# Optimization experiments

Hardware: AMD Instinct MI355X
Metric: run time of the kernel (lower is better)

Reference implementation:

```python
import jax, jax.numpy as jnp
import numpy as np

NUM_NODES = 500000
MEM_DIM = 172
BATCH = 4096


def setup_inputs() -> dict:
    key = jax.random.key(0)
    ks = jax.random.split(key, 8)
    s = 1.0 / np.sqrt(MEM_DIM)  # torch GRUCell init: U(-1/sqrt(hidden), 1/sqrt(hidden))
    return {
        "node_ids": jax.random.randint(ks[0], (BATCH,), 0, NUM_NODES),
        "messages": jax.random.normal(ks[1], (BATCH, MEM_DIM), dtype=jnp.float32),
        "timestamps": jax.random.uniform(ks[2], (BATCH,), dtype=jnp.float32),
        "memory": jax.random.normal(ks[3], (NUM_NODES, MEM_DIM), dtype=jnp.float32) * 0.1,
        "last_update": jnp.zeros((NUM_NODES,), dtype=jnp.float32),
        "w_ih": jax.random.uniform(ks[4], (3 * MEM_DIM, MEM_DIM), minval=-s, maxval=s, dtype=jnp.float32),
        "w_hh": jax.random.uniform(ks[5], (3 * MEM_DIM, MEM_DIM), minval=-s, maxval=s, dtype=jnp.float32),
        "b_ih": jax.random.uniform(ks[6], (3 * MEM_DIM,), minval=-s, maxval=s, dtype=jnp.float32),
        "b_hh": jax.random.uniform(ks[7], (3 * MEM_DIM,), minval=-s, maxval=s, dtype=jnp.float32),
    }


def _gru_cell(x, h, w_ih, w_hh, b_ih, b_hh):
    # torch.nn.GRUCell math. x, h: [B, D]; w_*: [3D, D]; b_*: [3D]
    gi = x @ w_ih.T + b_ih  # [B, 3D]
    gh = h @ w_hh.T + b_hh  # [B, 3D]
    i_r, i_z, i_n = jnp.split(gi, 3, axis=-1)
    h_r, h_z, h_n = jnp.split(gh, 3, axis=-1)
    r = jax.nn.sigmoid(i_r + h_r)
    z = jax.nn.sigmoid(i_z + h_z)
    n = jnp.tanh(i_n + r * h_n)
    return (1.0 - z) * n + z * h


def reference(node_ids, messages, timestamps, memory, last_update, w_ih, w_hh, b_ih, b_hh):
    # Gather current memory for the touched nodes
    current = memory[node_ids]  # [B, D]
    updated = _gru_cell(messages, current, w_ih, w_hh, b_ih, b_hh)  # [B, D]
    new_memory = memory.at[node_ids].set(updated)
    new_last_update = last_update.at[node_ids].set(timestamps)
    return new_memory, new_last_update
```

## Files before the change

### kernel.cpp

```cpp
#include <hip/hip_runtime.h>
#include <math.h>

#define D     172
#define D4    43
#define G3    516
#define RPB   8
#define TPB   256
#define NCOPY 2048
#define WT_HALF (43 * 516)
#define WT_F4   (2 * WT_HALF)

typedef float vfloat4 __attribute__((ext_vector_type(4)));

__global__ __launch_bounds__(256) void prep_kernel(const float* __restrict__ w_ih,
                                                   const float* __restrict__ w_hh,
                                                   float4* __restrict__ wt) {
    int idx = blockIdx.x * 256 + threadIdx.x;
    if (idx < WT_F4) {
        int m   = idx / WT_HALF;
        int rem = idx - m * WT_HALF;
        int k4  = rem / G3;
        int row = rem - k4 * G3;
        const float* src = m ? w_hh : w_ih;
        wt[idx] = *(const float4*)(src + (long)row * D + 4 * k4);
    }
}

__global__ __launch_bounds__(TPB) void copy_kernel(const vfloat4* __restrict__ mem4,
                                                   const vfloat4* __restrict__ lu4,
                                                   vfloat4* __restrict__ out4,
                                                   vfloat4* __restrict__ outlu4,
                                                   unsigned memf4, unsigned luf4) {
    const unsigned gid    = blockIdx.x * TPB + threadIdx.x;
    const unsigned stride = NCOPY * TPB;

    for (unsigned i0 = gid; i0 < memf4; i0 += 4u * stride) {
        unsigned i1 = i0 + stride, i2 = i0 + 2u * stride, i3 = i0 + 3u * stride;
        vfloat4 v0, v1, v2, v3;
        v0 = mem4[i0];
        if (i1 < memf4) v1 = mem4[i1];
        if (i2 < memf4) v2 = mem4[i2];
        if (i3 < memf4) v3 = mem4[i3];
        out4[i0] = v0;
        if (i1 < memf4) out4[i1] = v1;
        if (i2 < memf4) out4[i2] = v2;
        if (i3 < memf4) out4[i3] = v3;
    }
    if (gid < luf4) outlu4[gid] = lu4[gid];
}

__global__ __launch_bounds__(TPB) void gru_kernel(
    const int*   __restrict__ ids,  const float* __restrict__ msg,
    const float* __restrict__ ts,   const float* __restrict__ mem,
    const float* __restrict__ b_ih, const float* __restrict__ b_hh,
    const float4* __restrict__ wt,
    float* __restrict__ out_mem,    float* __restrict__ out_lu,
    int B) {

    __shared__ float4 sxh[2][RPB][D4];
    __shared__ int    s_id[RPB];
    __shared__ float  s_ts[RPB];
    __shared__ int    s_dup[RPB];

    const int tid  = threadIdx.x;
    const int base = blockIdx.x * RPB;

    if (tid < RPB) {
        s_id[tid]  = ids[base + tid];
        s_ts[tid]  = ts[base + tid];
        s_dup[tid] = 0;
    }
    __syncthreads();

    for (int it = tid; it < 2 * RPB * D4; it += TPB) {
        int which = it / (RPB * D4);
        int rem   = it - which * (RPB * D4);
        int r     = rem / D4;
        int k4    = rem - r * D4;
        const float* src = which ? (mem + (long)s_id[r] * D)
                                 : (msg + (long)(base + r) * D);
        ((float4*)sxh)[it] = *(const float4*)(src + 4 * k4);
    }
    for (int r = 0; r < RPB; ++r) {
        int my = s_id[r];
        for (int j = base + r + 1 + tid; j < B; j += TPB) {
            if (ids[j] == my) { s_dup[r] = 1; break; }
        }
    }
    __syncthreads();

    if (tid < D) {
        float acc[6][RPB];
        #pragma unroll
        for (int g = 0; g < 6; ++g)
            #pragma unroll
            for (int r = 0; r < RPB; ++r) acc[g][r] = 0.0f;

        const float4* wtB = wt + WT_HALF;
        for (int k4 = 0; k4 < D4; ++k4) {
            const int o = k4 * G3 + tid;
            float4 a0 = wt [o];
            float4 a1 = wt [o + D];
            float4 a2 = wt [o + 2 * D];
            float4 c0 = wtB[o];
            float4 c1 = wtB[o + D];
            float4 c2 = wtB[o + 2 * D];
            #pragma unroll
            for (int r = 0; r < RPB; ++r) {
                float4 xv = sxh[0][r][k4];
                float4 hv = sxh[1][r][k4];
                acc[0][r] += a0.x * xv.x + a0.y * xv.y + a0.z * xv.z + a0.w * xv.w;
                acc[1][r] += a1.x * xv.x + a1.y * xv.y + a1.z * xv.z + a1.w * xv.w;
                acc[2][r] += a2.x * xv.x + a2.y * xv.y + a2.z * xv.z + a2.w * xv.w;
                acc[3][r] += c0.x * hv.x + c0.y * hv.y + c0.z * hv.z + c0.w * hv.w;
                acc[4][r] += c1.x * hv.x + c1.y * hv.y + c1.z * hv.z + c1.w * hv.w;
                acc[5][r] += c2.x * hv.x + c2.y * hv.y + c2.z * hv.z + c2.w * hv.w;
            }
        }

        float bir = b_ih[tid], biz = b_ih[D + tid], bin_ = b_ih[2 * D + tid];
        float bhr = b_hh[tid], bhz = b_hh[D + tid], bhn  = b_hh[2 * D + tid];
        #pragma unroll
        for (int r = 0; r < RPB; ++r) {
            float i_r = acc[0][r] + bir;
            float i_z = acc[1][r] + biz;
            float i_n = acc[2][r] + bin_;
            float h_r = acc[3][r] + bhr;
            float h_z = acc[4][r] + bhz;
            float h_n = acc[5][r] + bhn;
            float rg = 1.0f / (1.0f + expf(-(i_r + h_r)));
            float zg = 1.0f / (1.0f + expf(-(i_z + h_z)));
            float ng = tanhf(i_n + rg * h_n);
            float hv = ((const float*)sxh[1][r])[tid];
            float outv = (1.0f - zg) * ng + zg * hv;
            if (!s_dup[r]) out_mem[(long)s_id[r] * D + tid] = outv;
        }
    }
    if (tid < RPB && !s_dup[tid]) out_lu[s_id[tid]] = s_ts[tid];
}

extern "C" void kernel_launch(void* const* d_in, const int* in_sizes, int n_in,
                              void* d_out, int out_size, void* d_ws, size_t ws_size,
                              hipStream_t stream) {
    const int*   node_ids    = (const int*)d_in[0];
    const float* messages    = (const float*)d_in[1];
    const float* timestamps  = (const float*)d_in[2];
    const float* memory      = (const float*)d_in[3];
    const float* last_update = (const float*)d_in[4];
    const float* w_ih        = (const float*)d_in[5];
    const float* w_hh        = (const float*)d_in[6];
    const float* b_ih        = (const float*)d_in[7];
    const float* b_hh        = (const float*)d_in[8];
    float* out = (float*)d_out;

    const int B = in_sizes[0];
    const int N = in_sizes[4];
    const long memf = (long)N * D;
    const unsigned memf4 = (unsigned)(memf / 4);
    const unsigned luf4  = (unsigned)(N / 4);

    float4* wt = (float4*)d_ws;

    prep_kernel<<<(WT_F4 + 255) / 256, 256, 0, stream>>>(w_ih, w_hh, wt);
    copy_kernel<<<NCOPY, TPB, 0, stream>>>((const vfloat4*)memory,
                                           (const vfloat4*)last_update,
                                           (vfloat4*)out,
                                           (vfloat4*)(out + memf),
                                           memf4, luf4);
    gru_kernel<<<B / RPB, TPB, 0, stream>>>(node_ids, messages, timestamps, memory,
                                            b_ih, b_hh, (const float4*)wt,
                                            out, out + memf, B);
}
```

Before: 225.1 us.

## Fuse GRU compute with bulk memory copy and scatter results in separate kernel

Runs the GRU matmul blocks and the large memory/last_update copy in one launch, so the compute-bound GRU work overlaps the bandwidth-bound copy instead of running after it. GRU outputs, ids, timestamps and duplicate flags go to a workspace, and a new scatter kernel writes them into the output after the copy finishes. The copy loop is simplified to a single strided load/store per iteration. A fallback path with a naive direct GRU kernel is added for when the workspace is too small. The cost is an extra kernel launch plus a round trip of the GRU results through global memory.

```diff
diff --git a/kernel.cpp b/kernel.cpp
--- a/kernel.cpp
+++ b/kernel.cpp
@@ -6,6 +6,7 @@
 #define G3    516
 #define RPB   8
 #define TPB   256
+#define NGRU  512
 #define NCOPY 2048
 #define WT_HALF (43 * 516)
 #define WT_F4   (2 * WT_HALF)
@@ -26,49 +27,29 @@
     }
 }
 
-__global__ __launch_bounds__(TPB) void copy_kernel(const vfloat4* __restrict__ mem4,
-                                                   const vfloat4* __restrict__ lu4,
-                                                   vfloat4* __restrict__ out4,
-                                                   vfloat4* __restrict__ outlu4,
-                                                   unsigned memf4, unsigned luf4) {
-    const unsigned gid    = blockIdx.x * TPB + threadIdx.x;
-    const unsigned stride = NCOPY * TPB;
-
-    for (unsigned i0 = gid; i0 < memf4; i0 += 4u * stride) {
-        unsigned i1 = i0 + stride, i2 = i0 + 2u * stride, i3 = i0 + 3u * stride;
-        vfloat4 v0, v1, v2, v3;
-        v0 = mem4[i0];
-        if (i1 < memf4) v1 = mem4[i1];
-        if (i2 < memf4) v2 = mem4[i2];
-        if (i3 < memf4) v3 = mem4[i3];
-        out4[i0] = v0;
-        if (i1 < memf4) out4[i1] = v1;
-        if (i2 < memf4) out4[i2] = v2;
-        if (i3 < memf4) out4[i3] = v3;
-    }
-    if (gid < luf4) outlu4[gid] = lu4[gid];
-}
-
-__global__ __launch_bounds__(TPB) void gru_kernel(
+__device__ __forceinline__ void gru_block(
+    int gblk,
     const int*   __restrict__ ids,  const float* __restrict__ msg,
     const float* __restrict__ ts,   const float* __restrict__ mem,
     const float* __restrict__ b_ih, const float* __restrict__ b_hh,
     const float4* __restrict__ wt,
-    float* __restrict__ out_mem,    float* __restrict__ out_lu,
+    float* __restrict__ gout, int* __restrict__ g_id,
+    float* __restrict__ g_ts, int* __restrict__ g_dup,
     int B) {
 
     __shared__ float4 sxh[2][RPB][D4];
     __shared__ int    s_id[RPB];
-    __shared__ float  s_ts[RPB];
     __shared__ int    s_dup[RPB];
 
     const int tid  = threadIdx.x;
-    const int base = blockIdx.x * RPB;
+    const int base = gblk * RPB;
 
     if (tid < RPB) {
-        s_id[tid]  = ids[base + tid];
-        s_ts[tid]  = ts[base + tid];
+        int id = ids[base + tid];
+        s_id[tid]  = id;
         s_dup[tid] = 0;
+        g_id[base + tid] = id;
+        g_ts[base + tid] = ts[base + tid];
     }
     __syncthreads();
 
@@ -88,6 +69,7 @@
         }
     }
     __syncthreads();
+    if (tid < RPB) g_dup[base + tid] = s_dup[tid];
 
     if (tid < D) {
         float acc[6][RPB];
@@ -132,11 +114,99 @@
             float zg = 1.0f / (1.0f + expf(-(i_z + h_z)));
             float ng = tanhf(i_n + rg * h_n);
             float hv = ((const float*)sxh[1][r])[tid];
-            float outv = (1.0f - zg) * ng + zg * hv;
-            if (!s_dup[r]) out_mem[(long)s_id[r] * D + tid] = outv;
-        }
-    }
-    if (tid < RPB && !s_dup[tid]) out_lu[s_id[tid]] = s_ts[tid];
+            gout[(long)(base + r) * D + tid] = (1.0f - zg) * ng + zg * hv;
+        }
+    }
+}
+
+__global__ __launch_bounds__(TPB) void fused_kernel(
+    const int*   __restrict__ ids,  const float* __restrict__ msg,
+    const float* __restrict__ ts,   const float* __restrict__ mem,
+    const float* __restrict__ lu,
+    const float* __restrict__ b_ih, const float* __restrict__ b_hh,
+    const float4* __restrict__ wt,
+    float* __restrict__ gout, int* __restrict__ g_id,
+    float* __restrict__ g_ts, int* __restrict__ g_dup,
+    float* __restrict__ out_mem,    float* __restrict__ out_lu,
+    int B, int N) {
+
+    if (blockIdx.x < NGRU) {
+        gru_block(blockIdx.x, ids, msg, ts, mem, b_ih, b_hh, wt,
+                  gout, g_id, g_ts, g_dup, B);
+        return;
+    }
+    const unsigned gid    = (blockIdx.x - NGRU) * TPB + threadIdx.x;
+    const unsigned stride = NCOPY * TPB;
+    const unsigned memf4  = (unsigned)N * D4;
+    const vfloat4* mem4 = (const vfloat4*)mem;
+    vfloat4* out4 = (vfloat4*)out_mem;
+    for (unsigned i = gid; i < memf4; i += stride) out4[i] = mem4[i];
+    const unsigned luf4 = (unsigned)N / 4;
+    const vfloat4* lu4 = (const vfloat4*)lu;
+    vfloat4* outlu4 = (vfloat4*)out_lu;
+    for (unsigned i = gid; i < luf4; i += stride) outlu4[i] = lu4[i];
+}
+
+__global__ __launch_bounds__(TPB) void scatter_kernel(
+    const float* __restrict__ gout, const int* __restrict__ g_id,
+    const float* __restrict__ g_ts, const int* __restrict__ g_dup,
+    float* __restrict__ out_mem, float* __restrict__ out_lu, int B) {
+    int idx = blockIdx.x * TPB + threadIdx.x;
+    int total = B * D;
+    if (idx < total) {
+        int r = idx / D;
+        int d = idx - r * D;
+        if (!g_dup[r]) out_mem[(long)g_id[r] * D + d] = gout[idx];
+    } else if (idx < total + B) {
+        int r = idx - total;
+        if (!g_dup[r]) out_lu[g_id[r]] = g_ts[r];
+    }
+}
+
+__global__ __launch_bounds__(TPB) void copy_kernel(const vfloat4* __restrict__ mem4,
+                                                   const vfloat4* __restrict__ lu4,
+                                                   vfloat4* __restrict__ out4,
+                                                   vfloat4* __restrict__ outlu4,
+                                                   unsigned memf4, unsigned luf4) {
+    const unsigned gid    = blockIdx.x * TPB + threadIdx.x;
+    const unsigned stride = NCOPY * TPB;
+    for (unsigned i = gid; i < memf4; i += stride) out4[i] = mem4[i];
+    for (unsigned i = gid; i < luf4; i += stride) outlu4[i] = lu4[i];
+}
+
+__global__ __launch_bounds__(TPB) void gru_direct_kernel(
+    const int*   __restrict__ ids,  const float* __restrict__ msg,
+    const float* __restrict__ ts,   const float* __restrict__ mem,
+    const float* __restrict__ w_ih, const float* __restrict__ w_hh,
+    const float* __restrict__ b_ih, const float* __restrict__ b_hh,
+    float* __restrict__ out_mem,    float* __restrict__ out_lu, int B) {
+    int r = blockIdx.x;
+    int tid = threadIdx.x;
+    __shared__ float sx[D], sh[D];
+    __shared__ int s_id, s_dup;
+    if (tid == 0) { s_id = ids[r]; s_dup = 0; }
+    __syncthreads();
+    if (tid < D) { sx[tid] = msg[(long)r * D + tid]; sh[tid] = mem[(long)s_id * D + tid]; }
+    for (int j = r + 1 + tid; j < B; j += TPB) if (ids[j] == s_id) { s_dup = 1; break; }
+    __syncthreads();
+    if (s_dup) return;
+    if (tid < D) {
+        float a[6] = {0,0,0,0,0,0};
+        for (int k = 0; k < D; ++k) {
+            float xv = sx[k], hv = sh[k];
+            a[0] += w_ih[(long)(0*D+tid)*D+k] * xv;
+            a[1] += w_ih[(long)(1*D+tid)*D+k] * xv;
+            a[2] += w_ih[(long)(2*D+tid)*D+k] * xv;
+            a[3] += w_hh[(long)(0*D+tid)*D+k] * hv;
+            a[4] += w_hh[(long)(1*D+tid)*D+k] * hv;
+            a[5] += w_hh[(long)(2*D+tid)*D+k] * hv;
+        }
+        float rg = 1.0f / (1.0f + expf(-(a[0] + b_ih[tid] + a[3] + b_hh[tid])));
+        float zg = 1.0f / (1.0f + expf(-(a[1] + b_ih[D+tid] + a[4] + b_hh[D+tid])));
+        float ng = tanhf(a[2] + b_ih[2*D+tid] + rg * (a[5] + b_hh[2*D+tid]));
+        out_mem[(long)s_id * D + tid] = (1.0f - zg) * ng + zg * sh[tid];
+    }
+    if (tid == 0) out_lu[s_id] = ts[r];
 }
 
 extern "C" void kernel_launch(void* const* d_in, const int* in_sizes, int n_in,
@@ -156,18 +226,36 @@
     const int B = in_sizes[0];
     const int N = in_sizes[4];
     const long memf = (long)N * D;
-    const unsigned memf4 = (unsigned)(memf / 4);
-    const unsigned luf4  = (unsigned)(N / 4);
-
-    float4* wt = (float4*)d_ws;
-
-    prep_kernel<<<(WT_F4 + 255) / 256, 256, 0, stream>>>(w_ih, w_hh, wt);
-    copy_kernel<<<NCOPY, TPB, 0, stream>>>((const vfloat4*)memory,
-                                           (const vfloat4*)last_update,
-                                           (vfloat4*)out,
-                                           (vfloat4*)(out + memf),
-                                           memf4, luf4);
-    gru_kernel<<<B / RPB, TPB, 0, stream>>>(node_ids, messages, timestamps, memory,
-                                            b_ih, b_hh, (const float4*)wt,
-                                            out, out + memf, B);
-}
+
+    size_t off_wt   = 0;
+    size_t off_gout = off_wt + (size_t)WT_F4 * 16;
+    size_t off_id   = off_gout + (size_t)B * D * 4;
+    size_t off_ts   = off_id + (size_t)B * 4;
+    size_t off_dup  = off_ts + (size_t)B * 4;
+    size_t ws_need  = off_dup + (size_t)B * 4;
+
+    if (ws_size >= ws_need) {
+        float4* wt    = (float4*)((char*)d_ws + off_wt);
+        float*  gout  = (float*)((char*)d_ws + off_gout);
+        int*    g_id  = (int*)((char*)d_ws + off_id);
+        float*  g_ts  = (float*)((char*)d_ws + off_ts);
+        int*    g_dup = (int*)((char*)d_ws + off_dup);
+
+        prep_kernel<<<(WT_F4 + 255) / 256, 256, 0, stream>>>(w_ih, w_hh, wt);
+        fused_kernel<<<NGRU + NCOPY, TPB, 0, stream>>>(
+            node_ids, messages, timestamps, memory, last_update,
+            b_ih, b_hh, (const float4*)wt,
+            gout, g_id, g_ts, g_dup, out, out + memf, B, N);
+        scatter_kernel<<<(B * D + B + TPB - 1) / TPB, TPB, 0, stream>>>(
+            gout, g_id, g_ts, g_dup, out, out + memf, B);
+    } else {
+        copy_kernel<<<NCOPY, TPB, 0, stream>>>((const vfloat4*)memory,
+                                               (const vfloat4*)last_update,
+                                               (vfloat4*)out,
+                                               (vfloat4*)(out + memf),
+                                               (unsigned)(memf / 4), (unsigned)(N / 4));
+        gru_direct_kernel<<<B, TPB, 0, stream>>>(node_ids, messages, timestamps, memory,
+                                                 w_ih, w_hh, b_ih, b_hh,
+                                                 out, out + memf, B);
+    }
+}
```

Result: faster. 218.6 us (-2.9%).
